# Performance work log

Hardware: AMD Instinct MI355X
Metric: run time of the kernel (lower is better)

Reference implementation:

```python
import jax, jax.numpy as jnp
import numpy as np

# pywt 'db4' decomposition filters
DEC_LO = np.array([-0.010597401784997278, 0.032883011666982945, 0.030841381835986965,
                   -0.18703481171888114, -0.02798376941698385, 0.6308807679295904,
                   0.7148465705525415, 0.23037781330885523], dtype=np.float32)
DEC_HI = np.array([(-1.0) ** (k + 1) * DEC_LO[len(DEC_LO) - 1 - k] for k in range(len(DEC_LO))],
                  dtype=np.float32)
FLEN = 8
LEVELS = 4
# lax conv does cross-correlation; pywt dwt is convolution -> reverse the filters.
# Kernel shape [out_ch=2 (lo,hi), in_ch=1, width=8]
KERNEL = jnp.stack([jnp.asarray(DEC_LO[::-1].copy()), jnp.asarray(DEC_HI[::-1].copy())])[:, None, :]


def _dwt_step(x):
    """One pywt-compatible DWT level with 'symmetric' extension.
    x: [N, 1, L] -> (cA [N,1,Lo], cD [N,1,Lo]) with Lo = floor((L+FLEN-1)/2).
    pywt: extend by FLEN-1 each side, full-conv, take every 2nd sample starting at 1.
    Equivalent: slice ext[1:], stride-2 valid cross-correlation with reversed filter."""
    ext = jnp.pad(x, ((0, 0), (0, 0), (FLEN - 1, FLEN - 1)), mode='symmetric')[:, :, 1:]
    out = jax.lax.conv_general_dilated(ext, KERNEL, window_strides=(2,), padding='VALID',
                                       dimension_numbers=('NCH', 'OIH', 'NCH'))
    return out[:, 0:1, :], out[:, 1:2, :]


def setup_inputs() -> dict:
    key = jax.random.key(0)
    trajectory = jax.random.normal(key, (16, 4096, 256), dtype=jnp.float32)
    return {"trajectory": trajectory}


def reference(trajectory) -> jnp.ndarray:
    """Batched multi-level DWT (pywt.wavedec, db4, symmetric, level=4),
    each coefficient band zero-padded to `timesteps`.
    Returns [batch, timesteps, levels+1, features]; band axis ordered
    [cA4, cD4, cD3, cD2, cD1] exactly as pywt.wavedec returns them.
    (Original torch code stored these values in a dict; values are identical.)"""
    B, T, F = trajectory.shape
    # vectorize all (batch, feature) signals together: [B*F, 1, T]
    x = trajectory.transpose(0, 2, 1).reshape(B * F, 1, T)
    details = []
    cur = x
    for _ in range(LEVELS):
        cur, cD = _dwt_step(cur)
        details.append(cD)
    bands = [cur] + details[::-1]  # [cA4, cD4, cD3, cD2, cD1]
    # zero-pad each band at the end to length T (matches _pad_coefficients)
    padded = [jnp.pad(c[:, 0, :], ((0, 0), (0, T - c.shape[-1]))) for c in bands]
    stacked = jnp.stack(padded, axis=1)  # [B*F, LEVELS+1, T]
    return stacked.reshape(B, F, LEVELS + 1, T).transpose(0, 3, 2, 1)  # [B, T, LEVELS+1, F]
```

## Files before the change

kernel.cpp:

```cpp
#include <hip/hip_runtime.h>


namespace {
constexpr int T_LEN = 4096;
constexpr int F_DIM = 256;
constexpr int NB    = 5;
constexpr int L1 = 2051, L2 = 1029, L3 = 518, L4 = 262;
}

typedef float f32x4 __attribute__((ext_vector_type(4)));

__device__ __constant__ float RLO[8] = {
     0.23037781330885523f,   0.7148465705525415f,   0.6308807679295904f,
    -0.02798376941698385f,  -0.18703481171888114f,  0.030841381835986965f,
     0.032883011666982945f, -0.010597401784997278f };

__device__ __constant__ float RHI[8] = {
    -0.010597401784997278f, -0.032883011666982945f, 0.030841381835986965f,
     0.18703481171888114f,  -0.02798376941698385f, -0.6308807679295904f,
     0.7148465705525415f,   -0.23037781330885523f };

__device__ __host__ constexpr int refl(int i, int L) {
    return (i < 0) ? (-1 - i) : ((i >= L) ? (2 * L - 1 - i) : i);
}

__device__ __forceinline__ void nt_store(float* p, float v) {
    __builtin_nontemporal_store(v, p);
}

template<int Z>
__device__ __forceinline__ void fill_zeros(float* __restrict__ outB,
                                           int t0, int t1, int tid)
{
    const f32x4 z4 = {0.f, 0.f, 0.f, 0.f};
    for (int t = t0; t < t1; ++t) {
        float* row = outB + (size_t)t * NB * F_DIM;
        #pragma unroll
        for (int c0 = 0; c0 < Z * F_DIM; c0 += 4 * F_DIM) {
            const int c = c0 + tid * 4;
            if (c < Z * F_DIM)
                __builtin_nontemporal_store(z4, (f32x4*)(row + c));
        }
    }
}

template<int KX>
__device__ __forceinline__ void cascade(const float* __restrict__ inb,
                                        float* __restrict__ outb, int krt)
{
    constexpr bool EX = (KX >= 0);
    constexpr bool DP = (KX == 65);
    constexpr int N1 = DP ? 82 : 74, N2 = DP ? 38 : 34, N3 = DP ? 16 : 14;
    constexpr int OWN1 = DP ? 50 : 42, OWN2 = DP ? 22 : 18, OWN3 = DP ? 8 : 6;
    constexpr int R1LO = (KX == 0) ? 42 : (KX == 1) ? 10 : 0;
    constexpr int R1HI = (KX == 64) ? 45 : (KX == 65) ? 21 : N1;
    constexpr int R2LO = (KX == 0) ? 18 : (KX == 1) ? 2 : 0;
    constexpr int R2HI = (KX == 64) ? 23 : (KX == 65) ? 11 : N2;
    constexpr int R3LO = (KX == 0) ? 6 : 0;
    constexpr int R3HI = (KX == 64) ? 12 : (KX == 65) ? 6 : N3;
    constexpr int MHI  = (KX == 65) ? 2 : 4;

    const int k   = EX ? KX : krt;
    const int t1b = 32 * k - (DP ? 50 : 42);
    const int t2b = 16 * k - (DP ? 22 : 18);
    const int t3b = 8 * k  - (DP ? 8  : 6);

    float A[N1], B[N2], C[N3];

    float xw[8];
    #pragma unroll
    for (int j = 0; j < 8; ++j) {
        int g = 2 * (t1b + R1LO) - 6 + j;
        if (EX) g = refl(g, T_LEN);
        xw[j] = inb[(size_t)g * F_DIM];
    }
    #pragma unroll
    for (int r1 = R1LO; r1 < R1HI; ++r1) {
        float a = 0.f, d = 0.f;
        #pragma unroll
        for (int j = 0; j < 8; ++j) { a = fmaf(xw[j], RLO[j], a); d = fmaf(xw[j], RHI[j], d); }
        A[r1] = a;
        const int t1 = t1b + r1;
        if (r1 >= OWN1)
            nt_store(outb + ((size_t)t1 * NB + 4) * F_DIM, d);
        if (r1 + 1 < R1HI) {
            #pragma unroll
            for (int j = 0; j < 6; ++j) xw[j] = xw[j + 2];
            int g6 = 2 * t1 + 2, g7 = 2 * t1 + 3;
            if (EX) { g6 = refl(g6, T_LEN); g7 = refl(g7, T_LEN); }
            xw[6] = inb[(size_t)g6 * F_DIM];
            xw[7] = inb[(size_t)g7 * F_DIM];
        }
    }

    #pragma unroll
    for (int r2 = R2LO; r2 < R2HI; ++r2) {
        float a = 0.f, d = 0.f;
        #pragma unroll
        for (int j = 0; j < 8; ++j) {
            const int i1 = EX ? (refl(2 * (t2b + r2) - 6 + j, L1) - t1b) : (2 * r2 + j);
            const float v = A[i1];
            a = fmaf(v, RLO[j], a); d = fmaf(v, RHI[j], d);
        }
        B[r2] = a;
        if (r2 >= OWN2)
            nt_store(outb + ((size_t)(t2b + r2) * NB + 3) * F_DIM, d);
    }

    #pragma unroll
    for (int r3 = R3LO; r3 < R3HI; ++r3) {
        float a = 0.f, d = 0.f;
        #pragma unroll
        for (int j = 0; j < 8; ++j) {
            const int i2 = EX ? (refl(2 * (t3b + r3) - 6 + j, L2) - t2b) : (2 * r3 + j);
            const float v = B[i2];
            a = fmaf(v, RLO[j], a); d = fmaf(v, RHI[j], d);
        }
        C[r3] = a;
        if (r3 >= OWN3)
            nt_store(outb + ((size_t)(t3b + r3) * NB + 2) * F_DIM, d);
    }

    #pragma unroll
    for (int m = 0; m < MHI; ++m) {
        float a = 0.f, d = 0.f;
        #pragma unroll
        for (int j = 0; j < 8; ++j) {
            const int i3 = EX ? (refl(2 * (4 * k + m) - 6 + j, L3) - t3b) : (2 * m + j);
            const float v = C[i3];
            a = fmaf(v, RLO[j], a); d = fmaf(v, RHI[j], d);
        }
        const int t4 = 4 * k + m;
        nt_store(outb + ((size_t)t4 * NB + 1) * F_DIM, d);
        nt_store(outb + ((size_t)t4 * NB + 0) * F_DIM, a);
    }
}

extern "C" __global__ __launch_bounds__(256)
void dwt_fused(const float* __restrict__ in, float* __restrict__ out)
{
    const int tid = threadIdx.x;
    const int per = gridDim.x >> 3;
    const int wg  = (int)(blockIdx.x & 7) * per + (int)(blockIdx.x >> 3);
    const int b   = wg >> 7;
    const int j   = wg & 127;

    float* outB = out + (size_t)b * T_LEN * NB * F_DIM;

    if (j < 66) {
        const float* inb = in + (size_t)b * T_LEN * F_DIM + tid;
        float* outb = outB + tid;
        switch (j) {
            case 0:  cascade<0 >(inb, outb, j); break;
            case 1:  cascade<1 >(inb, outb, j); break;
            case 64: cascade<64>(inb, outb, j); break;
            case 65: cascade<65>(inb, outb, j); break;
            default: cascade<-1>(inb, outb, j); break;
        }
    } else {
        const int slot = j - 66;
        if (slot < 2) {
            const int t0 = 262 + slot * 128;
            fill_zeros<2>(outB, t0, t0 + 128, tid);
        } else if (slot < 8) {
            const int i = slot - 2;
            const int t0 = 518 + i * 86;
            fill_zeros<3>(outB, t0, (t0 + 86 < L2) ? t0 + 86 : L2, tid);
        } else if (slot < 24) {
            const int i = slot - 8;
            const int t0 = 1029 + i * 64;
            fill_zeros<4>(outB, t0, (t0 + 64 < L1) ? t0 + 64 : L1, tid);
        } else {
            const int i = slot - 24;
            const int t0 = 2051 + i * 54;
            fill_zeros<5>(outB, t0, (t0 + 54 < T_LEN) ? t0 + 54 : T_LEN, tid);
        }
    }
}

extern "C" void kernel_launch(void* const* d_in, const int* in_sizes, int n_in,
                              void* d_out, int out_size, void* d_ws, size_t ws_size,
                              hipStream_t stream)
{
    const float* traj = (const float*)d_in[0];
    float* out = (float*)d_out;
    hipLaunchKernelGGL(dwt_fused, dim3(16 * 128), dim3(F_DIM), 0, stream, traj, out);
}
```

Measured before the change: 71.35 us.

## Split edge blocks into separate kernel and stream interior cascade with ring buffers

Interior tiles now compute all four DWT levels in one streaming pass, holding only 8-entry ring buffers per level instead of full A/B/C arrays. This cuts register pressure so launch bounds can request 6 waves per SIMD. The four reflection-handling edge tiles per batch move into a second small kernel, which removes the switch-heavy divergent code from the main kernel. The cost is a second kernel launch, plus a small serial tail where the edge kernel runs with very few blocks.

```diff
diff --git a/kernel.cpp b/kernel.cpp
--- a/kernel.cpp
+++ b/kernel.cpp
@@ -44,11 +44,84 @@
     }
 }
 
+__device__ __forceinline__ void cascade_interior(const float* __restrict__ inb,
+                                                 float* __restrict__ outb, int k)
+{
+    const int t1b = 32 * k - 42;
+    const int t2b = 16 * k - 18;
+    const int t3b = 8  * k - 6;
+
+    float xw[8], Aw[8], Bw[8], Cw[8];
+
+    #pragma unroll
+    for (int j = 0; j < 8; ++j)
+        xw[j] = inb[(size_t)(2 * t1b - 6 + j) * F_DIM];
+
+    #pragma unroll
+    for (int r1 = 0; r1 < 74; ++r1) {
+        float a1 = 0.f, d1 = 0.f;
+        #pragma unroll
+        for (int j = 0; j < 8; ++j) {
+            const float v = xw[(2 * r1 + j) & 7];
+            a1 = fmaf(v, RLO[j], a1);
+            d1 = fmaf(v, RHI[j], d1);
+        }
+        Aw[r1 & 7] = a1;
+        if (r1 >= 42)
+            nt_store(outb + ((size_t)(t1b + r1) * NB + 4) * F_DIM, d1);
+        if (r1 < 73) {
+            xw[(2 * r1 + 8) & 7] = inb[(size_t)(2 * (t1b + r1) + 2) * F_DIM];
+            xw[(2 * r1 + 9) & 7] = inb[(size_t)(2 * (t1b + r1) + 3) * F_DIM];
+        }
+
+        if ((r1 & 1) && r1 >= 7) {
+            const int r2 = (r1 - 7) >> 1;
+            float a2 = 0.f, d2 = 0.f;
+            #pragma unroll
+            for (int j = 0; j < 8; ++j) {
+                const float v = Aw[(2 * r2 + j) & 7];
+                a2 = fmaf(v, RLO[j], a2);
+                d2 = fmaf(v, RHI[j], d2);
+            }
+            Bw[r2 & 7] = a2;
+            if (r2 >= 18)
+                nt_store(outb + ((size_t)(t2b + r2) * NB + 3) * F_DIM, d2);
+
+            if ((r2 & 1) && r2 >= 7) {
+                const int r3 = (r2 - 7) >> 1;
+                float a3 = 0.f, d3 = 0.f;
+                #pragma unroll
+                for (int j = 0; j < 8; ++j) {
+                    const float v = Bw[(2 * r3 + j) & 7];
+                    a3 = fmaf(v, RLO[j], a3);
+                    d3 = fmaf(v, RHI[j], d3);
+                }
+                Cw[r3 & 7] = a3;
+                if (r3 >= 6)
+                    nt_store(outb + ((size_t)(t3b + r3) * NB + 2) * F_DIM, d3);
+
+                if ((r3 & 1) && r3 >= 7) {
+                    const int r4 = (r3 - 7) >> 1;
+                    float a4 = 0.f, d4 = 0.f;
+                    #pragma unroll
+                    for (int j = 0; j < 8; ++j) {
+                        const float v = Cw[(2 * r4 + j) & 7];
+                        a4 = fmaf(v, RLO[j], a4);
+                        d4 = fmaf(v, RHI[j], d4);
+                    }
+                    const int t4 = 4 * k + r4;
+                    nt_store(outb + ((size_t)t4 * NB + 1) * F_DIM, d4);
+                    nt_store(outb + ((size_t)t4 * NB + 0) * F_DIM, a4);
+                }
+            }
+        }
+    }
+}
+
 template<int KX>
 __device__ __forceinline__ void cascade(const float* __restrict__ inb,
-                                        float* __restrict__ outb, int krt)
-{
-    constexpr bool EX = (KX >= 0);
+                                        float* __restrict__ outb)
+{
     constexpr bool DP = (KX == 65);
     constexpr int N1 = DP ? 82 : 74, N2 = DP ? 38 : 34, N3 = DP ? 16 : 14;
     constexpr int OWN1 = DP ? 50 : 42, OWN2 = DP ? 22 : 18, OWN3 = DP ? 8 : 6;
@@ -60,18 +133,17 @@
     constexpr int R3HI = (KX == 64) ? 12 : (KX == 65) ? 6 : N3;
     constexpr int MHI  = (KX == 65) ? 2 : 4;
 
-    const int k   = EX ? KX : krt;
-    const int t1b = 32 * k - (DP ? 50 : 42);
-    const int t2b = 16 * k - (DP ? 22 : 18);
-    const int t3b = 8 * k  - (DP ? 8  : 6);
+    constexpr int k   = KX;
+    constexpr int t1b = 32 * k - (DP ? 50 : 42);
+    constexpr int t2b = 16 * k - (DP ? 22 : 18);
+    constexpr int t3b = 8 * k  - (DP ? 8  : 6);
 
     float A[N1], B[N2], C[N3];
 
     float xw[8];
     #pragma unroll
     for (int j = 0; j < 8; ++j) {
-        int g = 2 * (t1b + R1LO) - 6 + j;
-        if (EX) g = refl(g, T_LEN);
+        const int g = refl(2 * (t1b + R1LO) - 6 + j, T_LEN);
         xw[j] = inb[(size_t)g * F_DIM];
     }
     #pragma unroll
@@ -86,8 +158,7 @@
         if (r1 + 1 < R1HI) {
             #pragma unroll
             for (int j = 0; j < 6; ++j) xw[j] = xw[j + 2];
-            int g6 = 2 * t1 + 2, g7 = 2 * t1 + 3;
-            if (EX) { g6 = refl(g6, T_LEN); g7 = refl(g7, T_LEN); }
+            const int g6 = refl(2 * t1 + 2, T_LEN), g7 = refl(2 * t1 + 3, T_LEN);
             xw[6] = inb[(size_t)g6 * F_DIM];
             xw[7] = inb[(size_t)g7 * F_DIM];
         }
@@ -98,8 +169,7 @@
         float a = 0.f, d = 0.f;
         #pragma unroll
         for (int j = 0; j < 8; ++j) {
-            const int i1 = EX ? (refl(2 * (t2b + r2) - 6 + j, L1) - t1b) : (2 * r2 + j);
-            const float v = A[i1];
+            const float v = A[refl(2 * (t2b + r2) - 6 + j, L1) - t1b];
             a = fmaf(v, RLO[j], a); d = fmaf(v, RHI[j], d);
         }
         B[r2] = a;
@@ -112,8 +182,7 @@
         float a = 0.f, d = 0.f;
         #pragma unroll
         for (int j = 0; j < 8; ++j) {
-            const int i2 = EX ? (refl(2 * (t3b + r3) - 6 + j, L2) - t2b) : (2 * r3 + j);
-            const float v = B[i2];
+            const float v = B[refl(2 * (t3b + r3) - 6 + j, L2) - t2b];
             a = fmaf(v, RLO[j], a); d = fmaf(v, RHI[j], d);
         }
         C[r3] = a;
@@ -126,8 +195,7 @@
         float a = 0.f, d = 0.f;
         #pragma unroll
         for (int j = 0; j < 8; ++j) {
-            const int i3 = EX ? (refl(2 * (4 * k + m) - 6 + j, L3) - t3b) : (2 * m + j);
-            const float v = C[i3];
+            const float v = C[refl(2 * (4 * k + m) - 6 + j, L3) - t3b];
             a = fmaf(v, RLO[j], a); d = fmaf(v, RHI[j], d);
         }
         const int t4 = 4 * k + m;
@@ -136,29 +204,23 @@
     }
 }
 
-extern "C" __global__ __launch_bounds__(256)
-void dwt_fused(const float* __restrict__ in, float* __restrict__ out)
+extern "C" __global__ __launch_bounds__(256, 6)
+void dwt_interior(const float* __restrict__ in, float* __restrict__ out)
 {
     const int tid = threadIdx.x;
     const int per = gridDim.x >> 3;
     const int wg  = (int)(blockIdx.x & 7) * per + (int)(blockIdx.x >> 3);
-    const int b   = wg >> 7;
-    const int j   = wg & 127;
+    const int b   = wg / 124;
+    const int j   = wg % 124;
 
     float* outB = out + (size_t)b * T_LEN * NB * F_DIM;
 
-    if (j < 66) {
+    if (j < 62) {
+        const int k = j + 2;
         const float* inb = in + (size_t)b * T_LEN * F_DIM + tid;
-        float* outb = outB + tid;
-        switch (j) {
-            case 0:  cascade<0 >(inb, outb, j); break;
-            case 1:  cascade<1 >(inb, outb, j); break;
-            case 64: cascade<64>(inb, outb, j); break;
-            case 65: cascade<65>(inb, outb, j); break;
-            default: cascade<-1>(inb, outb, j); break;
-        }
+        cascade_interior(inb, outB + tid, k);
     } else {
-        const int slot = j - 66;
+        const int slot = j - 62;
         if (slot < 2) {
             const int t0 = 262 + slot * 128;
             fill_zeros<2>(outB, t0, t0 + 128, tid);
@@ -178,11 +240,30 @@
     }
 }
 
+extern "C" __global__ __launch_bounds__(256)
+void dwt_edge(const float* __restrict__ in, float* __restrict__ out)
+{
+    const int f   = threadIdx.x;
+    const int b   = (int)blockIdx.x >> 2;
+    const int sel = (int)blockIdx.x & 3;
+
+    const float* inb = in + (size_t)b * T_LEN * F_DIM + f;
+    float* outb = out + (size_t)b * T_LEN * NB * F_DIM + f;
+
+    switch (sel) {
+        case 0: cascade<0 >(inb, outb); break;
+        case 1: cascade<1 >(inb, outb); break;
+        case 2: cascade<64>(inb, outb); break;
+        case 3: cascade<65>(inb, outb); break;
+    }
+}
+
 extern "C" void kernel_launch(void* const* d_in, const int* in_sizes, int n_in,
                               void* d_out, int out_size, void* d_ws, size_t ws_size,
                               hipStream_t stream)
 {
     const float* traj = (const float*)d_in[0];
     float* out = (float*)d_out;
-    hipLaunchKernelGGL(dwt_fused, dim3(16 * 128), dim3(F_DIM), 0, stream, traj, out);
-}
+    hipLaunchKernelGGL(dwt_interior, dim3(16 * 124), dim3(F_DIM), 0, stream, traj, out);
+    hipLaunchKernelGGL(dwt_edge,     dim3(16 * 4),   dim3(F_DIM), 0, stream, traj, out);
+}
```

Result: slower. 92.00 us (+28.9%).
